# Kernel optimization log

Measured on AMD Instinct MI355X. Metric: run time of the kernel, lower is better.

The kernel has to match this reference:

```python
import jax, jax.numpy as jnp
import numpy as np

B, S, D, H = 2, 2048, 2048, 16
HD = D // H
EPS = 1e-5


def layernorm(x, scale, shift):
    mean = jnp.mean(x, axis=-1, keepdims=True)
    var = jnp.mean((x - mean) ** 2, axis=-1, keepdims=True)  # unbiased=False
    return scale * (x - mean) / jnp.sqrt(var + EPS) + shift


def gelu_buggy(x):
    # Faithful to source: tanh is applied ONLY to the constant sqrt(2/pi)
    c = jnp.tanh(jnp.sqrt(jnp.asarray(2.0 / jnp.pi, dtype=x.dtype)))
    return 0.5 * x * (1.0 + c * (x + 0.044715 * x ** 3))


def setup_inputs() -> dict:
    key = jax.random.key(0)
    ks = jax.random.split(key, 10)
    sd = 0.02
    return {
        "x": jax.random.normal(ks[0], (B, S, D), dtype=jnp.float32),
        "wq": jax.random.normal(ks[1], (D, D), dtype=jnp.float32) * sd,
        "wk": jax.random.normal(ks[2], (D, D), dtype=jnp.float32) * sd,
        "wv": jax.random.normal(ks[3], (D, D), dtype=jnp.float32) * sd,
        "wo": jax.random.normal(ks[4], (D, D), dtype=jnp.float32) * sd,
        "bo": jnp.zeros((D,), dtype=jnp.float32),
        "w1": jax.random.normal(ks[5], (D, 4 * D), dtype=jnp.float32) * sd,
        "b1": jnp.zeros((4 * D,), dtype=jnp.float32),
        "w2": jax.random.normal(ks[6], (4 * D, D), dtype=jnp.float32) * sd,
        "b2": jnp.zeros((D,), dtype=jnp.float32),
        "ln_scale": jnp.ones((D,), dtype=jnp.float32),
        "ln_shift": jnp.zeros((D,), dtype=jnp.float32),
    }


def attention(h, wq, wk, wv, wo, bo):
    b, s, _ = h.shape
    q = (h @ wq).reshape(b, s, H, HD).transpose(0, 2, 1, 3)  # [b,h,s,hd]
    k = (h @ wk).reshape(b, s, H, HD).transpose(0, 2, 1, 3)
    v = (h @ wv).reshape(b, s, H, HD).transpose(0, 2, 1, 3)
    scores = jnp.einsum('bhqd,bhkd->bhqk', q, k)
    causal = jnp.tril(jnp.ones((s, s), dtype=bool))
    scores = jnp.where(causal, scores, -jnp.inf)
    w = jax.nn.softmax(scores / jnp.sqrt(jnp.asarray(HD, dtype=h.dtype)), axis=-1)
    ctx = jnp.einsum('bhqk,bhkd->bhqd', w, v).transpose(0, 2, 1, 3).reshape(b, s, D)
    return ctx @ wo + bo


def reference(x, wq, wk, wv, wo, bo, w1, b1, w2, b2, ln_scale, ln_shift):
    # NB: source applies ln1 before BOTH sub-blocks (ln2 unused); dropout is identity (p=0 / eval)
    shortcut = x
    h = layernorm(x, ln_scale, ln_shift)
    h = attention(h, wq, wk, wv, wo, bo)
    x = h + shortcut
    shortcut = x
    h = layernorm(x, ln_scale, ln_shift)
    h = gelu_buggy(h @ w1 + b1) @ w2 + b2
    return h + shortcut
```

## Files before the change

### kernel.cpp

```cpp
#include <hip/hip_runtime.h>
#include <hip/hip_bf16.h>
#include <math.h>


typedef short bf16x8 __attribute__((ext_vector_type(8)));
typedef float f32x4 __attribute__((ext_vector_type(4)));
typedef short short4v __attribute__((ext_vector_type(4)));

#define MFMA16x32(a, b, c) __builtin_amdgcn_mfma_f32_16x16x32_bf16((a), (b), (c), 0, 0, 0)

__device__ __forceinline__ short f2bs(float f) {
    unsigned u = __builtin_bit_cast(unsigned, f);
    unsigned r = (u + 0x7FFFu + ((u >> 16) & 1u)) >> 16;
    return (short)(unsigned short)r;
}

__device__ __forceinline__ float bs2f(short s) {
    unsigned u = ((unsigned)(unsigned short)s) << 16;
    return __builtin_bit_cast(float, u);
}

__device__ __forceinline__ void gload_lds16(const void* g, void* l) {
    __builtin_amdgcn_global_load_lds(
        (const __attribute__((address_space(1))) unsigned int*)g,
        (__attribute__((address_space(3))) unsigned int*)l, 16, 0, 0);
}

template <int N>
__device__ __forceinline__ void vmw() {
    if constexpr (N == 0) asm volatile("s_waitcnt vmcnt(0)" ::: "memory");
    else if constexpr (N == 3) asm volatile("s_waitcnt vmcnt(3)" ::: "memory");
    else if constexpr (N == 6) asm volatile("s_waitcnt vmcnt(6)" ::: "memory");
    else if constexpr (N == 12) asm volatile("s_waitcnt vmcnt(12)" ::: "memory");
}

__global__ __launch_bounds__(256) void transpose_all_kernel(
    const float* __restrict__ wq, const float* __restrict__ wk,
    const float* __restrict__ wv, const float* __restrict__ wo,
    const float* __restrict__ w1, const float* __restrict__ w2,
    short* __restrict__ wqkvT, short* __restrict__ woT,
    short* __restrict__ w1T, short* __restrict__ w2T) {
    const int D = 2048;
    __shared__ float tile[32][33];
    int blk = blockIdx.x;
    const float* in;
    short* out;
    int R, C, bx, by;
    if (blk < 16384) {
        int r = blk >> 12;
        in = (r == 0) ? wq : (r == 1) ? wk : (r == 2) ? wv : wo;
        out = (r < 3) ? (wqkvT + (size_t)r * D * D) : woT;
        R = D; C = D;
        int lb = blk & 4095; bx = lb & 63; by = lb >> 6;
    } else if (blk < 32768) {
        in = w1; out = w1T; R = D; C = 4 * D;
        int lb = blk - 16384; bx = lb & 255; by = lb >> 8;
    } else {
        in = w2; out = w2T; R = 4 * D; C = D;
        int lb = blk - 32768; bx = lb & 63; by = lb >> 6;
    }
    const int tx = threadIdx.x & 31;
    const int ty = threadIdx.x >> 5;
    const int c0 = bx * 32, r0 = by * 32;
#pragma unroll
    for (int i = 0; i < 4; ++i) {
        int r = ty + i * 8;
        tile[r][tx] = in[(size_t)(r0 + r) * C + c0 + tx];
    }
    __syncthreads();
#pragma unroll
    for (int i = 0; i < 4; ++i) {
        int r = ty + i * 8;
        out[(size_t)(c0 + r) * R + r0 + tx] = f2bs(tile[tx][r]);
    }
}

__global__ __launch_bounds__(256) void ln_kernel(const float* __restrict__ x,
                                                 const float* __restrict__ sc,
                                                 const float* __restrict__ sh,
                                                 short* __restrict__ out) {
    const int D = 2048;
    const int row = blockIdx.x;
    const int tid = threadIdx.x;
    __shared__ float red[4];
    const float4* xr = (const float4*)(x + (size_t)row * D);
    float4 v0 = xr[tid];
    float4 v1 = xr[tid + 256];
    float vals0[4] = {v0.x, v0.y, v0.z, v0.w};
    float vals1[4] = {v1.x, v1.y, v1.z, v1.w};

    float s = vals0[0] + vals0[1] + vals0[2] + vals0[3] + vals1[0] + vals1[1] + vals1[2] + vals1[3];
#pragma unroll
    for (int off = 32; off; off >>= 1) s += __shfl_xor(s, off);
    if ((tid & 63) == 0) red[tid >> 6] = s;
    __syncthreads();
    float mean = (red[0] + red[1] + red[2] + red[3]) * (1.0f / 2048.0f);
    __syncthreads();

    float q = 0.0f;
#pragma unroll
    for (int j = 0; j < 4; ++j) {
        float t0 = vals0[j] - mean;
        float t1 = vals1[j] - mean;
        q += t0 * t0 + t1 * t1;
    }
#pragma unroll
    for (int off = 32; off; off >>= 1) q += __shfl_xor(q, off);
    if ((tid & 63) == 0) red[tid >> 6] = q;
    __syncthreads();
    float var = (red[0] + red[1] + red[2] + red[3]) * (1.0f / 2048.0f);
    float inv = rsqrtf(var + 1e-5f);

    const int c0 = tid * 4;
    const int c1 = (tid + 256) * 4;
    short4v o0, o1;
#pragma unroll
    for (int j = 0; j < 4; ++j) {
        o0[j] = f2bs(sc[c0 + j] * ((vals0[j] - mean) * inv) + sh[c0 + j]);
        o1[j] = f2bs(sc[c1 + j] * ((vals1[j] - mean) * inv) + sh[c1 + j]);
    }
    *(short4v*)(out + (size_t)row * D + c0) = o0;
    *(short4v*)(out + (size_t)row * D + c1) = o1;
}

__global__ __launch_bounds__(256) void ln_bf16_kernel(const short* __restrict__ x,
                                                      const float* __restrict__ sc,
                                                      const float* __restrict__ sh,
                                                      short* __restrict__ out) {
    const int D = 2048;
    const int row = blockIdx.x;
    const int tid = threadIdx.x;
    __shared__ float red[4];
    bf16x8 v = *(const bf16x8*)(x + (size_t)row * D + tid * 8);
    float vals[8];
#pragma unroll
    for (int j = 0; j < 8; ++j) vals[j] = bs2f(v[j]);

    float s = 0.f;
#pragma unroll
    for (int j = 0; j < 8; ++j) s += vals[j];
#pragma unroll
    for (int off = 32; off; off >>= 1) s += __shfl_xor(s, off);
    if ((tid & 63) == 0) red[tid >> 6] = s;
    __syncthreads();
    float mean = (red[0] + red[1] + red[2] + red[3]) * (1.0f / 2048.0f);
    __syncthreads();

    float q = 0.0f;
#pragma unroll
    for (int j = 0; j < 8; ++j) {
        float t = vals[j] - mean;
        q += t * t;
    }
#pragma unroll
    for (int off = 32; off; off >>= 1) q += __shfl_xor(q, off);
    if ((tid & 63) == 0) red[tid >> 6] = q;
    __syncthreads();
    float var = (red[0] + red[1] + red[2] + red[3]) * (1.0f / 2048.0f);
    float inv = rsqrtf(var + 1e-5f);

    const int c0 = tid * 8;
    bf16x8 o;
#pragma unroll
    for (int j = 0; j < 8; ++j)
        o[j] = f2bs(sc[c0 + j] * ((vals[j] - mean) * inv) + sh[c0 + j]);
    *(bf16x8*)(out + (size_t)row * D + c0) = o;
}

template <int EPI>
__global__ __launch_bounds__(512, 1) void gemm3d(const short* __restrict__ A,
                                                 const short* __restrict__ Bt,
                                                 int M, int N, int K,
                                                 void* __restrict__ Cout,
                                                 const float* __restrict__ bias,
                                                 const float* __restrict__ res,
                                                 float gconst) {
    extern __shared__ __align__(16) short lds[];
    const int tid = threadIdx.x;
    const int lane = tid & 63;
    const int wid = tid >> 6;
    const int wm = wid >> 1, wn = wid & 1;
    const int l15 = lane & 15, grp = lane >> 4;

    const int gx = gridDim.x;
    int flat = (int)blockIdx.y * gx + (int)blockIdx.x;
    const int cpx = (gx * (int)gridDim.y) >> 3;
    flat = (flat & 7) * cpx + (flat >> 3);
    const int bx = flat % gx, by = flat / gx;
    const long m0 = (long)by * 256, n0 = (long)bx * 128;

    f32x4 zero = {0.f, 0.f, 0.f, 0.f};
    f32x4 acc[4][4];
#pragma unroll
    for (int i = 0; i < 4; i++)
#pragma unroll
        for (int j = 0; j < 4; j++) acc[i][j] = zero;

    auto STAGE = [&](long k0, int b) {
        short* bufA = lds + b * 24576;
        short* bufB = bufA + 16384;
#pragma unroll
        for (int j = 0; j < 4; ++j) {
            int c = tid + j * 512;
            int row = c >> 3, sl = (c & 7) ^ (row & 7);
            gload_lds16(A + (size_t)(m0 + row) * K + k0 + sl * 8,
                        bufA + (size_t)(wid * 64 + j * 512) * 8);
        }
#pragma unroll
        for (int j = 0; j < 2; ++j) {
            int c = tid + j * 512;
            int row = c >> 3, sl = (c & 7) ^ (row & 7);
            gload_lds16(Bt + (size_t)(n0 + row) * K + k0 + sl * 8,
                        bufB + (size_t)(wid * 64 + j * 512) * 8);
        }
    };

    const int nt = K >> 6;
    STAGE(0, 0);
    STAGE(64, 1);
    int cur = 0, nx2 = 2;

    for (int t = 0; t < nt; ++t) {
        if (t + 2 < nt) {
            STAGE((long)(t + 2) * 64, nx2);
            vmw<12>();
        } else if (t + 1 < nt) {
            vmw<6>();
        } else {
            vmw<0>();
        }
        __builtin_amdgcn_s_barrier();
        __builtin_amdgcn_sched_barrier(0);

        const short* bufA = lds + cur * 24576;
        const short* bufB = bufA + 16384;
        bf16x8 af[2][4], bfr[2][4];
#pragma unroll
        for (int kk = 0; kk < 2; ++kk) {
#pragma unroll
            for (int m = 0; m < 4; ++m) {
                int row = wm * 64 + m * 16 + l15;
                af[kk][m] = *(const bf16x8*)(bufA + row * 64 + (((kk * 4 + grp) ^ (row & 7)) * 8));
            }
#pragma unroll
            for (int n = 0; n < 4; ++n) {
                int row = wn * 64 + n * 16 + l15;
                bfr[kk][n] = *(const bf16x8*)(bufB + row * 64 + (((kk * 4 + grp) ^ (row & 7)) * 8));
            }
        }
        __builtin_amdgcn_s_setprio(1);
#pragma unroll
        for (int kk = 0; kk < 2; ++kk)
#pragma unroll
            for (int m = 0; m < 4; ++m)
#pragma unroll
                for (int n = 0; n < 4; ++n)
                    acc[m][n] = MFMA16x32(af[kk][m], bfr[kk][n], acc[m][n]);
        __builtin_amdgcn_s_setprio(0);
        asm volatile("s_waitcnt lgkmcnt(0)" ::: "memory");
        __builtin_amdgcn_s_barrier();
        __builtin_amdgcn_sched_barrier(0);
        cur = (cur == 2) ? 0 : cur + 1;
        nx2 = (nx2 == 2) ? 0 : nx2 + 1;
    }

#pragma unroll
    for (int m = 0; m < 4; m++) {
        long gr = m0 + wm * 64 + m * 16 + grp * 4;
#pragma unroll
        for (int n = 0; n < 4; n++) {
            long gcol = n0 + wn * 64 + n * 16 + l15;
#pragma unroll
            for (int r = 0; r < 4; r++) {
                float vv = acc[m][n][r];
                long idx = (gr + r) * N + gcol;
                if constexpr (EPI == 0) {
                    ((short*)Cout)[idx] = f2bs(vv);
                } else if constexpr (EPI == 1) {
                    ((float*)Cout)[idx] = vv + bias[gcol] + res[idx];
                } else if constexpr (EPI == 2) {
                    float t2 = vv + bias[gcol];
                    float g = 0.5f * t2 * (1.0f + gconst * (t2 + 0.044715f * t2 * t2 * t2));
                    ((short*)Cout)[idx] = f2bs(g);
                } else if constexpr (EPI == 3) {
                    ((short*)Cout)[idx] = f2bs(vv + bias[gcol] + res[idx]);
                } else {
                    ((float*)Cout)[idx] = vv + bias[gcol] + bs2f(((const short*)res)[idx]);
                }
            }
        }
    }
}

template <int EPI>
__global__ __launch_bounds__(512, 4) void gemm3b(const short* __restrict__ A,
                                                 const short* __restrict__ Bt,
                                                 int M, int N, int K,
                                                 void* __restrict__ Cout,
                                                 const float* __restrict__ bias,
                                                 const float* __restrict__ res,
                                                 float gconst) {
    extern __shared__ __align__(16) short lds[];
    const int tid = threadIdx.x;
    const int lane = tid & 63;
    const int wid = tid >> 6;
    const int wm = wid >> 1, wn = wid & 1;
    const int l15 = lane & 15, grp = lane >> 4;

    const int gx = gridDim.x;
    int flat = (int)blockIdx.y * gx + (int)blockIdx.x;
    const int cpx = (gx * (int)gridDim.y) >> 3;
    flat = (flat & 7) * cpx + (flat >> 3);
    const int bx = flat % gx, by = flat / gx;
    const long m0 = (long)by * 256, n0 = (long)bx * 128;

    f32x4 zero = {0.f, 0.f, 0.f, 0.f};
    f32x4 acc[4][4];
#pragma unroll
    for (int i = 0; i < 4; i++)
#pragma unroll
        for (int j = 0; j < 4; j++) acc[i][j] = zero;

    auto STAGE = [&](int t, int b) {
        short* bufA = lds + b * 12288;
        short* bufB = bufA + 8192;
        const long k0 = (long)t << 5;
#pragma unroll
        for (int j = 0; j < 2; ++j) {
            int c = tid + j * 512;
            int row = c >> 2, sl = (c & 3) ^ ((row ^ (row >> 2)) & 3);
            gload_lds16(A + (size_t)(m0 + row) * K + k0 + sl * 8, bufA + (size_t)c * 8);
        }
        {
            int c = tid;
            int row = c >> 2, sl = (c & 3) ^ ((row ^ (row >> 2)) & 3);
            gload_lds16(Bt + (size_t)(n0 + row) * K + k0 + sl * 8, bufB + (size_t)c * 8);
        }
    };

    const int nt = K >> 5;
    STAGE(0, 0);
    STAGE(1, 1);
    int cur = 0, nx2 = 2;

    for (int t = 0; t < nt; ++t) {
        if (t + 2 < nt) {
            STAGE(t + 2, nx2);
            vmw<6>();
        } else if (t + 1 < nt) {
            vmw<3>();
        } else {
            vmw<0>();
        }
        __builtin_amdgcn_s_barrier();
        __builtin_amdgcn_sched_barrier(0);

        const short* bufA = lds + cur * 12288;
        const short* bufB = bufA + 8192;
        bf16x8 af[4], bfr[4];
#pragma unroll
        for (int m = 0; m < 4; ++m) {
            int row = wm * 64 + m * 16 + l15;
            af[m] = *(const bf16x8*)(bufA + row * 32 + (((grp ^ (row ^ (row >> 2))) & 3) * 8));
        }
#pragma unroll
        for (int n = 0; n < 4; ++n) {
            int row = wn * 64 + n * 16 + l15;
            bfr[n] = *(const bf16x8*)(bufB + row * 32 + (((grp ^ (row ^ (row >> 2))) & 3) * 8));
        }
        __builtin_amdgcn_s_setprio(1);
#pragma unroll
        for (int m = 0; m < 4; ++m)
#pragma unroll
            for (int n = 0; n < 4; ++n)
                acc[m][n] = MFMA16x32(af[m], bfr[n], acc[m][n]);
        __builtin_amdgcn_s_setprio(0);
        asm volatile("s_waitcnt lgkmcnt(0)" ::: "memory");
        __builtin_amdgcn_s_barrier();
        __builtin_amdgcn_sched_barrier(0);
        cur = (cur == 2) ? 0 : cur + 1;
        nx2 = (nx2 == 2) ? 0 : nx2 + 1;
    }

#pragma unroll
    for (int m = 0; m < 4; m++) {
        long gr = m0 + wm * 64 + m * 16 + grp * 4;
#pragma unroll
        for (int n = 0; n < 4; n++) {
            long gcol = n0 + wn * 64 + n * 16 + l15;
#pragma unroll
            for (int r = 0; r < 4; r++) {
                float vv = acc[m][n][r];
                long idx = (gr + r) * N + gcol;
                if constexpr (EPI == 0) {
                    ((short*)Cout)[idx] = f2bs(vv);
                } else if constexpr (EPI == 2) {
                    float t2 = vv + bias[gcol];
                    float g = 0.5f * t2 * (1.0f + gconst * (t2 + 0.044715f * t2 * t2 * t2));
                    ((short*)Cout)[idx] = f2bs(g);
                } else {
                    ((float*)Cout)[idx] = vv + bias[gcol] + res[idx];
                }
            }
        }
    }
}

__global__ __launch_bounds__(256) void reshape_v_kernel(const short* __restrict__ qkv,
                                                        short* __restrict__ Vt) {
    __shared__ short tile[32][33];
    const int bid = blockIdx.x;
    const int dt = bid & 3, st = (bid >> 2) & 63, bh = bid >> 8;
    const int b = bh >> 4, h = bh & 15;
    const int s0 = st * 32, d0 = dt * 32;
    const int tx = threadIdx.x & 31, ty = threadIdx.x >> 5;
#pragma unroll
    for (int i = 0; i < 4; ++i) {
        int s = ty + i * 8;
        tile[s][tx] = qkv[(size_t)(b * 2048 + s0 + s) * 6144 + 4096 + h * 128 + d0 + tx];
    }
    __syncthreads();
#pragma unroll
    for (int i = 0; i < 4; ++i) {
        int d = ty + i * 8;
        Vt[((size_t)bh * 128 + d0 + d) * 2048 + s0 + tx] = tile[tx][d];
    }
}

__global__ __launch_bounds__(256) void flash3_kernel(const short* __restrict__ qp,
                                                     const short* __restrict__ Vt,
                                                     short* __restrict__ ctx) {
    const int S = 2048, D = 2048, HD = 128, LD = 6144;
    __shared__ __align__(16) short Ks[2][64 * 128];
    __shared__ __align__(16) short Vs[2][64 * 128];
    __shared__ __align__(16) short Ps[4][16 * 64];
    const int tid = threadIdx.x;
    const int lane = tid & 63, wid = tid >> 6;
    const int l15 = lane & 15, grp = lane >> 4;

    int bid = (int)blockIdx.x;
    bid = (bid & 7) * 64 + (bid >> 3);
    const int p = bid & 15, bh = bid >> 4;
    const int b = bh >> 4, h = bh & 15;
    const int qtH = 31 - p;
    const int nH = qtH + 1;
    const float scale = 0.08838834764831845f;
    const float NEGINF = -__builtin_inff();

    const short* Kbase = qp + (size_t)b * S * LD + 2048 + (size_t)h * HD;
    const short* Vbase = Vt + (size_t)bh * 128 * S;
    short* Psw = &Ps[wid][0];

    f32x4 zero = {0.f, 0.f, 0.f, 0.f};
    bf16x8 aq[4];
    float m_[4], l_[4];
    f32x4 o[8];

    int qt = qtH;
    int qw = qt * 64 + wid * 16;
    {
        const short* qrow = qp + (size_t)(b * S + qw + l15) * LD + h * HD;
#pragma unroll
        for (int kc = 0; kc < 4; kc++) aq[kc] = *(const bf16x8*)(qrow + kc * 32 + grp * 8);
    }
#pragma unroll
    for (int r = 0; r < 4; r++) { m_[r] = NEGINF; l_[r] = 0.f; }
#pragma unroll
    for (int n = 0; n < 8; n++) o[n] = zero;

#pragma unroll
    for (int j = 0; j < 4; ++j) {
        int c = tid + j * 256;
        int r = c >> 4, sl = c & 15;
        gload_lds16(Kbase + (size_t)r * LD + ((sl ^ (r & 7)) * 8),
                    Ks[0] + (size_t)(wid * 64 + j * 256) * 8);
    }
#pragma unroll
    for (int j = 0; j < 4; ++j) {
        int c = tid + j * 256;
        int d = c >> 3, sl = c & 7;
        gload_lds16(Vbase + (size_t)d * S + ((sl ^ (d & 7)) * 8),
                    Vs[0] + (size_t)(wid * 64 + j * 256) * 8);
    }
    __syncthreads();

    int cur = 0;
    for (int i = 0; i < 33; ++i) {
        const int kt = (i < nH) ? i : (i - nH);
        const bool lastT = (kt == qt);

        if (i + 1 < 33) {
            const int ktn = (i + 1 < nH) ? (i + 1) : (i + 1 - nH);
            const long kn0 = (long)ktn * 64;
            const short* Kg = Kbase + (size_t)kn0 * LD;
            const short* Vg = Vbase + kn0;
            short* kd = Ks[cur ^ 1];
            short* vd = Vs[cur ^ 1];
#pragma unroll
            for (int j = 0; j < 4; ++j) {
                int c = tid + j * 256;
                int r = c >> 4, sl = c & 15;
                gload_lds16(Kg + (size_t)r * LD + ((sl ^ (r & 7)) * 8),
                            kd + (size_t)(wid * 64 + j * 256) * 8);
            }
#pragma unroll
            for (int j = 0; j < 4; ++j) {
                int c = tid + j * 256;
                int d = c >> 3, sl = c & 7;
                gload_lds16(Vg + (size_t)d * S + ((sl ^ (d & 7)) * 8),
                            vd + (size_t)(wid * 64 + j * 256) * 8);
            }
        }

        const short* Kc = Ks[cur];
        const short* Vc = Vs[cur];

        f32x4 s[4] = {zero, zero, zero, zero};
#pragma unroll
        for (int n = 0; n < 4; ++n) {
            int r = n * 16 + l15;
#pragma unroll
            for (int kc = 0; kc < 4; ++kc) {
                bf16x8 kb = *(const bf16x8*)(Kc + r * 128 + (((kc * 4 + grp) ^ (r & 7)) * 8));
                s[n] = MFMA16x32(aq[kc], kb, s[n]);
            }
        }

        float al[4];
#pragma unroll
        for (int r = 0; r < 4; ++r) {
            float v[4];
#pragma unroll
            for (int n = 0; n < 4; ++n) v[n] = s[n][r] * scale;
            if (lastT) {
                int qrel = wid * 16 + grp * 4 + r;
#pragma unroll
                for (int n = 0; n < 4; ++n)
                    if (n * 16 + l15 > qrel) v[n] = NEGINF;
            }
            float mx = fmaxf(fmaxf(v[0], v[1]), fmaxf(v[2], v[3]));
            mx = fmaxf(mx, __shfl_xor(mx, 1));
            mx = fmaxf(mx, __shfl_xor(mx, 2));
            mx = fmaxf(mx, __shfl_xor(mx, 4));
            mx = fmaxf(mx, __shfl_xor(mx, 8));
            float mn = fmaxf(m_[r], mx);
            float sc_ = __expf(m_[r] - mn);
            float rs = 0.f;
            int q = grp * 4 + r;
#pragma unroll
            for (int n = 0; n < 4; ++n) {
                v[n] = __expf(v[n] - mn);
                rs += v[n];
                Psw[q * 64 + (((n * 2 + (l15 >> 3)) ^ (q & 7)) * 8) + (l15 & 7)] = f2bs(v[n]);
            }
            rs += __shfl_xor(rs, 1);
            rs += __shfl_xor(rs, 2);
            rs += __shfl_xor(rs, 4);
            rs += __shfl_xor(rs, 8);
            l_[r] = l_[r] * sc_ + rs;
            m_[r] = mn;
            al[r] = sc_;
        }
#pragma unroll
        for (int n = 0; n < 8; n++) {
            f32x4 t = o[n];
            t[0] *= al[0]; t[1] *= al[1]; t[2] *= al[2]; t[3] *= al[3];
            o[n] = t;
        }

        bf16x8 pa[2];
#pragma unroll
        for (int kc = 0; kc < 2; ++kc)
            pa[kc] = *(const bf16x8*)(Psw + l15 * 64 + (((kc * 4 + grp) ^ (l15 & 7)) * 8));
#pragma unroll
        for (int n = 0; n < 8; ++n) {
            int d = n * 16 + l15;
#pragma unroll
            for (int kc = 0; kc < 2; ++kc) {
                bf16x8 vb = *(const bf16x8*)(Vc + d * 64 + (((kc * 4 + grp) ^ (d & 7)) * 8));
                o[n] = MFMA16x32(pa[kc], vb, o[n]);
            }
        }

        if (lastT) {
            float inv[4];
#pragma unroll
            for (int r = 0; r < 4; ++r) inv[r] = 1.0f / l_[r];
            short* cb_ = ctx + (size_t)(b * S + qw + grp * 4) * D + h * HD + l15;
#pragma unroll
            for (int n = 0; n < 8; ++n)
#pragma unroll
                for (int r = 0; r < 4; ++r)
                    cb_[(size_t)r * D + n * 16] = f2bs(o[n][r] * inv[r]);
            if (i < 32) {
                qt = 31 - qtH;
                qw = qt * 64 + wid * 16;
                const short* qrow = qp + (size_t)(b * S + qw + l15) * LD + h * HD;
#pragma unroll
                for (int kc = 0; kc < 4; kc++) aq[kc] = *(const bf16x8*)(qrow + kc * 32 + grp * 8);
#pragma unroll
                for (int r = 0; r < 4; r++) { m_[r] = NEGINF; l_[r] = 0.f; }
#pragma unroll
                for (int n = 0; n < 8; n++) o[n] = zero;
            }
        }
        __syncthreads();
        cur ^= 1;
    }
}

extern "C" void kernel_launch(void* const* d_in, const int* in_sizes, int n_in,
                              void* d_out, int out_size, void* d_ws, size_t ws_size,
                              hipStream_t stream) {
    const float* x    = (const float*)d_in[0];
    const float* wq   = (const float*)d_in[1];
    const float* wk   = (const float*)d_in[2];
    const float* wv   = (const float*)d_in[3];
    const float* wo   = (const float*)d_in[4];
    const float* bo   = (const float*)d_in[5];
    const float* w1   = (const float*)d_in[6];
    const float* b1   = (const float*)d_in[7];
    const float* w2   = (const float*)d_in[8];
    const float* b2   = (const float*)d_in[9];
    const float* lnsc = (const float*)d_in[10];
    const float* lnsh = (const float*)d_in[11];

    const int B = 2, S = 2048, D = 2048;
    const int M = B * S;
    const int LDS_3D = 3 * 24576 * 2;
    const int LDS_3B = 3 * 12288 * 2;

    char* p = (char*)d_ws;
    short* wqkvT = (short*)p; p += (size_t)3 * D * D * 2;
    short* woT   = (short*)p; p += (size_t)D * D * 2;
    short* w1T   = (short*)p; p += (size_t)4 * D * D * 2;
    short* w2T   = (short*)p; p += (size_t)4 * D * D * 2;
    short* lnb   = (short*)p; p += (size_t)M * D * 2;
    short* qkvb  = (short*)p;
    short* h1    = qkvb;
    p += (size_t)M * 3 * D * 2;
    short* ctxb  = (short*)p; p += (size_t)M * D * 2;
    short* x2    = (short*)p; p += (size_t)M * D * 2;

    short* Vt = x2;

    const float gconst = tanhf(sqrtf(2.0f / 3.14159265358979323846f));

    hipFuncSetAttribute((const void*)&gemm3d<0>, hipFuncAttributeMaxDynamicSharedMemorySize, LDS_3D);
    hipFuncSetAttribute((const void*)&gemm3d<3>, hipFuncAttributeMaxDynamicSharedMemorySize, LDS_3D);
    hipFuncSetAttribute((const void*)&gemm3d<4>, hipFuncAttributeMaxDynamicSharedMemorySize, LDS_3D);
    hipFuncSetAttribute((const void*)&gemm3b<2>, hipFuncAttributeMaxDynamicSharedMemorySize, LDS_3B);

    dim3 blk(256);
    transpose_all_kernel<<<dim3(49152), blk, 0, stream>>>(
        wq, wk, wv, wo, w1, w2, wqkvT, woT, w1T, w2T);

    ln_kernel<<<dim3(M), blk, 0, stream>>>(x, lnsc, lnsh, lnb);
    gemm3d<0><<<dim3(3 * D / 128, M / 256), dim3(512), LDS_3D, stream>>>(
        lnb, wqkvT, M, 3 * D, D, qkvb, nullptr, nullptr, 0.f);

    reshape_v_kernel<<<dim3(8192), blk, 0, stream>>>(qkvb, Vt);

    flash3_kernel<<<dim3(512), blk, 0, stream>>>(qkvb, Vt, ctxb);

    gemm3d<3><<<dim3(D / 128, M / 256), dim3(512), LDS_3D, stream>>>(
        ctxb, woT, M, D, D, x2, bo, x, 0.f);
    ln_bf16_kernel<<<dim3(M), blk, 0, stream>>>(x2, lnsc, lnsh, lnb);
    gemm3b<2><<<dim3(4 * D / 128, M / 256), dim3(512), LDS_3B, stream>>>(
        lnb, w1T, M, 4 * D, D, h1, b1, nullptr, gconst);
    gemm3d<4><<<dim3(D / 128, M / 256), dim3(512), LDS_3D, stream>>>(
        h1, w2T, M, D, 4 * D, (float*)d_out, b2, (const float*)x2, 0.f);
}
```

Measured before the change: 625.7 us.

## Replace 256x128 GEMM with 128x128 double-buffered kernel and raise flash MFMA priority

Removes the gemm3d kernel (256x128 tiles, 512 threads, triple-buffered, 1 block/CU). The QKV projection now uses the existing gemm3b, whose LDS footprint is smaller. The two N=2048 projections (wo and w2) use a new gemm2c kernel with 128x128 tiles, 256 threads, double buffering and 2 blocks per CU. The point is to give the narrow-N GEMMs more blocks and better occupancy, since 256x128 tiles only produced 128 blocks. The flash attention MFMA loops also get s_setprio raised. The trade-off is shallower prefetch and lower per-block reuse in gemm2c.

```diff
diff --git a/kernel.cpp b/kernel.cpp
--- a/kernel.cpp
+++ b/kernel.cpp
@@ -31,7 +31,7 @@
     if constexpr (N == 0) asm volatile("s_waitcnt vmcnt(0)" ::: "memory");
     else if constexpr (N == 3) asm volatile("s_waitcnt vmcnt(3)" ::: "memory");
     else if constexpr (N == 6) asm volatile("s_waitcnt vmcnt(6)" ::: "memory");
-    else if constexpr (N == 12) asm volatile("s_waitcnt vmcnt(12)" ::: "memory");
+    else if constexpr (N == 8) asm volatile("s_waitcnt vmcnt(8)" ::: "memory");
 }
 
 __global__ __launch_bounds__(256) void transpose_all_kernel(
@@ -168,131 +168,6 @@
 }
 
 template <int EPI>
-__global__ __launch_bounds__(512, 1) void gemm3d(const short* __restrict__ A,
-                                                 const short* __restrict__ Bt,
-                                                 int M, int N, int K,
-                                                 void* __restrict__ Cout,
-                                                 const float* __restrict__ bias,
-                                                 const float* __restrict__ res,
-                                                 float gconst) {
-    extern __shared__ __align__(16) short lds[];
-    const int tid = threadIdx.x;
-    const int lane = tid & 63;
-    const int wid = tid >> 6;
-    const int wm = wid >> 1, wn = wid & 1;
-    const int l15 = lane & 15, grp = lane >> 4;
-
-    const int gx = gridDim.x;
-    int flat = (int)blockIdx.y * gx + (int)blockIdx.x;
-    const int cpx = (gx * (int)gridDim.y) >> 3;
-    flat = (flat & 7) * cpx + (flat >> 3);
-    const int bx = flat % gx, by = flat / gx;
-    const long m0 = (long)by * 256, n0 = (long)bx * 128;
-
-    f32x4 zero = {0.f, 0.f, 0.f, 0.f};
-    f32x4 acc[4][4];
-#pragma unroll
-    for (int i = 0; i < 4; i++)
-#pragma unroll
-        for (int j = 0; j < 4; j++) acc[i][j] = zero;
-
-    auto STAGE = [&](long k0, int b) {
-        short* bufA = lds + b * 24576;
-        short* bufB = bufA + 16384;
-#pragma unroll
-        for (int j = 0; j < 4; ++j) {
-            int c = tid + j * 512;
-            int row = c >> 3, sl = (c & 7) ^ (row & 7);
-            gload_lds16(A + (size_t)(m0 + row) * K + k0 + sl * 8,
-                        bufA + (size_t)(wid * 64 + j * 512) * 8);
-        }
-#pragma unroll
-        for (int j = 0; j < 2; ++j) {
-            int c = tid + j * 512;
-            int row = c >> 3, sl = (c & 7) ^ (row & 7);
-            gload_lds16(Bt + (size_t)(n0 + row) * K + k0 + sl * 8,
-                        bufB + (size_t)(wid * 64 + j * 512) * 8);
-        }
-    };
-
-    const int nt = K >> 6;
-    STAGE(0, 0);
-    STAGE(64, 1);
-    int cur = 0, nx2 = 2;
-
-    for (int t = 0; t < nt; ++t) {
-        if (t + 2 < nt) {
-            STAGE((long)(t + 2) * 64, nx2);
-            vmw<12>();
-        } else if (t + 1 < nt) {
-            vmw<6>();
-        } else {
-            vmw<0>();
-        }
-        __builtin_amdgcn_s_barrier();
-        __builtin_amdgcn_sched_barrier(0);
-
-        const short* bufA = lds + cur * 24576;
-        const short* bufB = bufA + 16384;
-        bf16x8 af[2][4], bfr[2][4];
-#pragma unroll
-        for (int kk = 0; kk < 2; ++kk) {
-#pragma unroll
-            for (int m = 0; m < 4; ++m) {
-                int row = wm * 64 + m * 16 + l15;
-                af[kk][m] = *(const bf16x8*)(bufA + row * 64 + (((kk * 4 + grp) ^ (row & 7)) * 8));
-            }
-#pragma unroll
-            for (int n = 0; n < 4; ++n) {
-                int row = wn * 64 + n * 16 + l15;
-                bfr[kk][n] = *(const bf16x8*)(bufB + row * 64 + (((kk * 4 + grp) ^ (row & 7)) * 8));
-            }
-        }
-        __builtin_amdgcn_s_setprio(1);
-#pragma unroll
-        for (int kk = 0; kk < 2; ++kk)
-#pragma unroll
-            for (int m = 0; m < 4; ++m)
-#pragma unroll
-                for (int n = 0; n < 4; ++n)
-                    acc[m][n] = MFMA16x32(af[kk][m], bfr[kk][n], acc[m][n]);
-        __builtin_amdgcn_s_setprio(0);
-        asm volatile("s_waitcnt lgkmcnt(0)" ::: "memory");
-        __builtin_amdgcn_s_barrier();
-        __builtin_amdgcn_sched_barrier(0);
-        cur = (cur == 2) ? 0 : cur + 1;
-        nx2 = (nx2 == 2) ? 0 : nx2 + 1;
-    }
-
-#pragma unroll
-    for (int m = 0; m < 4; m++) {
-        long gr = m0 + wm * 64 + m * 16 + grp * 4;
-#pragma unroll
-        for (int n = 0; n < 4; n++) {
-            long gcol = n0 + wn * 64 + n * 16 + l15;
-#pragma unroll
-            for (int r = 0; r < 4; r++) {
-                float vv = acc[m][n][r];
-                long idx = (gr + r) * N + gcol;
-                if constexpr (EPI == 0) {
-                    ((short*)Cout)[idx] = f2bs(vv);
-                } else if constexpr (EPI == 1) {
-                    ((float*)Cout)[idx] = vv + bias[gcol] + res[idx];
-                } else if constexpr (EPI == 2) {
-                    float t2 = vv + bias[gcol];
-                    float g = 0.5f * t2 * (1.0f + gconst * (t2 + 0.044715f * t2 * t2 * t2));
-                    ((short*)Cout)[idx] = f2bs(g);
-                } else if constexpr (EPI == 3) {
-                    ((short*)Cout)[idx] = f2bs(vv + bias[gcol] + res[idx]);
-                } else {
-                    ((float*)Cout)[idx] = vv + bias[gcol] + bs2f(((const short*)res)[idx]);
-                }
-            }
-        }
-    }
-}
-
-template <int EPI>
 __global__ __launch_bounds__(512, 4) void gemm3b(const short* __restrict__ A,
                                                  const short* __restrict__ Bt,
                                                  int M, int N, int K,
@@ -394,12 +269,117 @@
                 long idx = (gr + r) * N + gcol;
                 if constexpr (EPI == 0) {
                     ((short*)Cout)[idx] = f2bs(vv);
-                } else if constexpr (EPI == 2) {
+                } else {
                     float t2 = vv + bias[gcol];
                     float g = 0.5f * t2 * (1.0f + gconst * (t2 + 0.044715f * t2 * t2 * t2));
                     ((short*)Cout)[idx] = f2bs(g);
+                }
+            }
+        }
+    }
+}
+
+template <int EPI>
+__global__ __launch_bounds__(256, 2) void gemm2c(const short* __restrict__ A,
+                                                 const short* __restrict__ Bt,
+                                                 int M, int N, int K,
+                                                 void* __restrict__ Cout,
+                                                 const float* __restrict__ bias,
+                                                 const float* __restrict__ res,
+                                                 float gconst) {
+    extern __shared__ __align__(16) short lds[];
+    const int tid = threadIdx.x;
+    const int lane = tid & 63;
+    const int wid = tid >> 6;
+    const int wm = wid >> 1, wn = wid & 1;
+    const int l15 = lane & 15, grp = lane >> 4;
+
+    const int gx = gridDim.x;
+    int flat = (int)blockIdx.y * gx + (int)blockIdx.x;
+    const int cpx = (gx * (int)gridDim.y) >> 3;
+    flat = (flat & 7) * cpx + (flat >> 3);
+    const int bx = flat % gx, by = flat / gx;
+    const long m0 = (long)by * 128, n0 = (long)bx * 128;
+
+    f32x4 zero = {0.f, 0.f, 0.f, 0.f};
+    f32x4 acc[4][4];
+#pragma unroll
+    for (int i = 0; i < 4; i++)
+#pragma unroll
+        for (int j = 0; j < 4; j++) acc[i][j] = zero;
+
+    auto STAGE = [&](int t, int b) {
+        short* bufA = lds + b * 16384;
+        short* bufB = bufA + 8192;
+        const long k0 = (long)t << 6;
+#pragma unroll
+        for (int j = 0; j < 4; ++j) {
+            int c = tid + j * 256;
+            int row = c >> 3, sl = (c & 7) ^ (row & 7);
+            gload_lds16(A + (size_t)(m0 + row) * K + k0 + sl * 8, bufA + (size_t)c * 8);
+        }
+#pragma unroll
+        for (int j = 0; j < 4; ++j) {
+            int c = tid + j * 256;
+            int row = c >> 3, sl = (c & 7) ^ (row & 7);
+            gload_lds16(Bt + (size_t)(n0 + row) * K + k0 + sl * 8, bufB + (size_t)c * 8);
+        }
+    };
+
+    const int nt = K >> 6;
+    STAGE(0, 0);
+    STAGE(1, 1);
+
+    for (int t = 0; t < nt; ++t) {
+        if (t + 1 < nt) { vmw<8>(); } else { vmw<0>(); }
+        __builtin_amdgcn_s_barrier();
+        __builtin_amdgcn_sched_barrier(0);
+
+        const short* bufA = lds + (t & 1) * 16384;
+        const short* bufB = bufA + 8192;
+        bf16x8 af[2][4], bfr[2][4];
+#pragma unroll
+        for (int kk = 0; kk < 2; ++kk) {
+#pragma unroll
+            for (int m = 0; m < 4; ++m) {
+                int row = wm * 64 + m * 16 + l15;
+                af[kk][m] = *(const bf16x8*)(bufA + row * 64 + (((kk * 4 + grp) ^ (row & 7)) * 8));
+            }
+#pragma unroll
+            for (int n = 0; n < 4; ++n) {
+                int row = wn * 64 + n * 16 + l15;
+                bfr[kk][n] = *(const bf16x8*)(bufB + row * 64 + (((kk * 4 + grp) ^ (row & 7)) * 8));
+            }
+        }
+        __builtin_amdgcn_s_setprio(1);
+#pragma unroll
+        for (int kk = 0; kk < 2; ++kk)
+#pragma unroll
+            for (int m = 0; m < 4; ++m)
+#pragma unroll
+                for (int n = 0; n < 4; ++n)
+                    acc[m][n] = MFMA16x32(af[kk][m], bfr[kk][n], acc[m][n]);
+        __builtin_amdgcn_s_setprio(0);
+        asm volatile("s_waitcnt lgkmcnt(0)" ::: "memory");
+        __builtin_amdgcn_s_barrier();
+        __builtin_amdgcn_sched_barrier(0);
+        if (t + 2 < nt) STAGE(t + 2, t & 1);
+    }
+
+#pragma unroll
+    for (int m = 0; m < 4; m++) {
+        long gr = m0 + wm * 64 + m * 16 + grp * 4;
+#pragma unroll
+        for (int n = 0; n < 4; n++) {
+            long gcol = n0 + wn * 64 + n * 16 + l15;
+#pragma unroll
+            for (int r = 0; r < 4; r++) {
+                float vv = acc[m][n][r];
+                long idx = (gr + r) * N + gcol;
+                if constexpr (EPI == 3) {
+                    ((short*)Cout)[idx] = f2bs(vv + bias[gcol] + res[idx]);
                 } else {
-                    ((float*)Cout)[idx] = vv + bias[gcol] + res[idx];
+                    ((float*)Cout)[idx] = vv + bias[gcol] + bs2f(((const short*)res)[idx]);
                 }
             }
         }
@@ -516,6 +496,7 @@
         const short* Vc = Vs[cur];
 
         f32x4 s[4] = {zero, zero, zero, zero};
+        __builtin_amdgcn_s_setprio(1);
 #pragma unroll
         for (int n = 0; n < 4; ++n) {
             int r = n * 16 + l15;
@@ -525,6 +506,7 @@
                 s[n] = MFMA16x32(aq[kc], kb, s[n]);
             }
         }
+        __builtin_amdgcn_s_setprio(0);
 
         float al[4];
 #pragma unroll
@@ -572,6 +554,7 @@
 #pragma unroll
         for (int kc = 0; kc < 2; ++kc)
             pa[kc] = *(const bf16x8*)(Psw + l15 * 64 + (((kc * 4 + grp) ^ (l15 & 7)) * 8));
+        __builtin_amdgcn_s_setprio(1);
 #pragma unroll
         for (int n = 0; n < 8; ++n) {
             int d = n * 16 + l15;
@@ -581,6 +564,7 @@
                 o[n] = MFMA16x32(pa[kc], vb, o[n]);
             }
         }
+        __builtin_amdgcn_s_setprio(0);
 
         if (lastT) {
             float inv[4];
@@ -627,8 +611,8 @@
 
     const int B = 2, S = 2048, D = 2048;
     const int M = B * S;
-    const int LDS_3D = 3 * 24576 * 2;
     const int LDS_3B = 3 * 12288 * 2;
+    const int LDS_2C = 2 * 16384 * 2;
 
     char* p = (char*)d_ws;
     short* wqkvT = (short*)p; p += (size_t)3 * D * D * 2;
@@ -646,28 +630,28 @@
 
     const float gconst = tanhf(sqrtf(2.0f / 3.14159265358979323846f));
 
-    hipFuncSetAttribute((const void*)&gemm3d<0>, hipFuncAttributeMaxDynamicSharedMemorySize, LDS_3D);
-    hipFuncSetAttribute((const void*)&gemm3d<3>, hipFuncAttributeMaxDynamicSharedMemorySize, LDS_3D);
-    hipFuncSetAttribute((const void*)&gemm3d<4>, hipFuncAttributeMaxDynamicSharedMemorySize, LDS_3D);
+    hipFuncSetAttribute((const void*)&gemm3b<0>, hipFuncAttributeMaxDynamicSharedMemorySize, LDS_3B);
     hipFuncSetAttribute((const void*)&gemm3b<2>, hipFuncAttributeMaxDynamicSharedMemorySize, LDS_3B);
+    hipFuncSetAttribute((const void*)&gemm2c<3>, hipFuncAttributeMaxDynamicSharedMemorySize, LDS_2C);
+    hipFuncSetAttribute((const void*)&gemm2c<4>, hipFuncAttributeMaxDynamicSharedMemorySize, LDS_2C);
 
     dim3 blk(256);
     transpose_all_kernel<<<dim3(49152), blk, 0, stream>>>(
         wq, wk, wv, wo, w1, w2, wqkvT, woT, w1T, w2T);
 
     ln_kernel<<<dim3(M), blk, 0, stream>>>(x, lnsc, lnsh, lnb);
-    gemm3d<0><<<dim3(3 * D / 128, M / 256), dim3(512), LDS_3D, stream>>>(
+    gemm3b<0><<<dim3(3 * D / 128, M / 256), dim3(512), LDS_3B, stream>>>(
         lnb, wqkvT, M, 3 * D, D, qkvb, nullptr, nullptr, 0.f);
 
     reshape_v_kernel<<<dim3(8192), blk, 0, stream>>>(qkvb, Vt);
 
     flash3_kernel<<<dim3(512), blk, 0, stream>>>(qkvb, Vt, ctxb);
 
-    gemm3d<3><<<dim3(D / 128, M / 256), dim3(512), LDS_3D, stream>>>(
+    gemm2c<3><<<dim3(D / 128, M / 128), blk, LDS_2C, stream>>>(
         ctxb, woT, M, D, D, x2, bo, x, 0.f);
     ln_bf16_kernel<<<dim3(M), blk, 0, stream>>>(x2, lnsc, lnsh, lnb);
     gemm3b<2><<<dim3(4 * D / 128, M / 256), dim3(512), LDS_3B, stream>>>(
         lnb, w1T, M, 4 * D, D, h1, b1, nullptr, gconst);
-    gemm3d<4><<<dim3(D / 128, M / 256), dim3(512), LDS_3D, stream>>>(
+    gemm2c<4><<<dim3(D / 128, M / 128), blk, LDS_2C, stream>>>(
         h1, w2T, M, D, 4 * D, (float*)d_out, b2, (const float*)x2, 0.f);
 }
```

Result: faster. 600.6 us (-4.0%).
